# Optimization experiments

Hardware: AMD Instinct MI355X
Metric: run time of the kernel (lower is better)

Reference implementation:

```python
import jax, jax.numpy as jnp
import numpy as np

E = 320000          # num edges
G = 256             # num graphs
NNF = 128           # node features
NEF = 64            # edge features
NGF = 64            # global features
HID = 128           # hidden channels
TGT = 64            # num targets
IN_CH = 2 * NNF + NEF + NGF  # 384


def setup_inputs() -> dict:
    key = jax.random.key(0)
    ks = jax.random.split(key, 10)
    ek = jax.random.normal(ks[0], (E, NEF), dtype=jnp.float32)
    vrk = jax.random.normal(ks[1], (E, NNF), dtype=jnp.float32)
    vsk = jax.random.normal(ks[2], (E, NNF), dtype=jnp.float32)
    u = jax.random.normal(ks[3], (G, NGF), dtype=jnp.float32)
    batch = jnp.sort(jax.random.randint(ks[4], (E,), 0, G, dtype=jnp.int64))
    # MLP params (Linear stores weight [out, in]; we keep [in, out] for x @ W)
    s1 = 1.0 / np.sqrt(IN_CH)
    s2 = 1.0 / np.sqrt(HID)
    W1 = jax.random.uniform(ks[5], (IN_CH, HID), jnp.float32, -s1, s1)
    b1 = jax.random.uniform(ks[6], (HID,), jnp.float32, -s1, s1)
    W2 = jax.random.uniform(ks[7], (HID, TGT), jnp.float32, -s2, s2)
    b2 = jax.random.uniform(ks[8], (TGT,), jnp.float32, -s2, s2)
    return {"ek": ek, "vrk": vrk, "vsk": vsk, "u": u, "batch": batch,
            "W1": W1, "b1": b1, "W2": W2, "b2": b2}


def reference(ek, vrk, vsk, u, batch, W1, b1, W2, b2):
    # gather per-edge global features, concat, 2-layer MLP with ReLU
    x = jnp.concatenate([ek, vrk, vsk, u[batch]], axis=1)  # [E, IN_CH]
    h = jax.nn.relu(x @ W1 + b1)                           # [E, HID]
    return h @ W2 + b2                                     # [E, TGT]
```

## Files before the change

kernel.cpp:

```cpp
#include <hip/hip_runtime.h>
#include <hip/hip_bf16.h>
#include <stdint.h>


typedef __bf16 bf16;
typedef __attribute__((ext_vector_type(8))) __bf16 bf16x8;
typedef __attribute__((ext_vector_type(4))) __bf16 bf16x4;
typedef __attribute__((ext_vector_type(4))) float floatx4;

__device__ __forceinline__ bf16x8 cvt_b8(floatx4 a, floatx4 b) {
  bf16x8 r;
  r[0] = (bf16)a.x; r[1] = (bf16)a.y; r[2] = (bf16)a.z; r[3] = (bf16)a.w;
  r[4] = (bf16)b.x; r[5] = (bf16)b.y; r[6] = (bf16)b.z; r[7] = (bf16)b.w;
  return r;
}
__device__ __forceinline__ bf16x4 cvt_b4(floatx4 v) {
  bf16x4 r;
  r[0] = (bf16)v.x; r[1] = (bf16)v.y; r[2] = (bf16)v.z; r[3] = (bf16)v.w;
  return r;
}

__global__ void pack_pre(const float* __restrict__ W1, bf16* __restrict__ w1p,
                         const float* __restrict__ W2, bf16* __restrict__ w2p) {
  int b = blockIdx.x, lane = threadIdx.x;
  int mm = lane & 15, qq = lane >> 4;
  if (b < 96) {
    int kc = b >> 3, hf = b & 7;
    bf16x8 r;
    #pragma unroll
    for (int j = 0; j < 8; ++j)
      r[j] = (bf16)W1[(kc * 32 + qq * 8 + j) * 128 + hf * 16 + mm];
    *(bf16x8*)(w1p + ((long)b * 64 + lane) * 8) = r;
  } else {
    int bb = b - 96;
    int ks = bb >> 2, tf = bb & 3;
    bf16x8 r;
    #pragma unroll
    for (int j = 0; j < 8; ++j)
      r[j] = (bf16)W2[(ks * 32 + qq * 8 + j) * 64 + tf * 16 + mm];
    *(bf16x8*)(w2p + ((long)bb * 64 + lane) * 8) = r;
  }
}

__global__ __launch_bounds__(256, 4) void edge_mlp(
    const float* __restrict__ ek, const float* __restrict__ vrk, const float* __restrict__ vsk,
    const float* __restrict__ u, const int* __restrict__ batch,
    const bf16* __restrict__ w1p, const float* __restrict__ b1,
    const bf16* __restrict__ w2p, const float* __restrict__ b2,
    float* __restrict__ out)
{
  __shared__ __align__(16) bf16 smem[16384];
  const int tid  = threadIdx.x;
  const int lane = tid & 63;
  const int wv   = tid >> 6;
  const int m    = lane & 15;
  const int q    = lane >> 4;
  bf16* hs = smem + wv * 4096;

  const int e0 = blockIdx.x * 128 + wv * 32;

  const float* px[4][2];
  #pragma unroll
  for (int ef = 0; ef < 2; ++ef) {
    int e = e0 + ef * 16 + m;
    px[0][ef] = ek  + (long)e * 64  + q * 8;
    px[1][ef] = vrk + (long)e * 128 + q * 8;
    px[2][ef] = vsk + (long)e * 128 + q * 8;
    px[3][ef] = u   + (long)batch[e] * 64 + q * 8;
  }
  const bf16* wp = w1p + lane * 8;

  floatx4 acc[8][2] = {};
  #pragma unroll
  for (int kc = 0; kc < 12; ++kc) {
    const int src = (kc < 2) ? 0 : (kc < 6) ? 1 : (kc < 10) ? 2 : 3;
    const int off = (kc < 2) ? kc * 32
                  : (kc < 6) ? (kc - 2) * 32
                  : (kc < 10) ? (kc - 6) * 32 : (kc - 10) * 32;
    bf16x8 xb[2];
    #pragma unroll
    for (int ef = 0; ef < 2; ++ef) {
      floatx4 v0 = *(const floatx4*)(px[src][ef] + off);
      floatx4 v1 = *(const floatx4*)(px[src][ef] + off + 4);
      xb[ef] = cvt_b8(v0, v1);
    }
    #pragma unroll
    for (int hf = 0; hf < 8; ++hf) {
      bf16x8 af = *(const bf16x8*)(wp + (kc * 8 + hf) * 512);
      acc[hf][0] = __builtin_amdgcn_mfma_f32_16x16x32_bf16(af, xb[0], acc[hf][0], 0, 0, 0);
      acc[hf][1] = __builtin_amdgcn_mfma_f32_16x16x32_bf16(af, xb[1], acc[hf][1], 0, 0, 0);
    }
  }

  #pragma unroll
  for (int hf = 0; hf < 8; ++hf) {
    floatx4 b1v = *(const floatx4*)(b1 + hf * 16 + q * 4);
    #pragma unroll
    for (int ef = 0; ef < 2; ++ef) {
      floatx4 v = acc[hf][ef] + b1v;
      v.x = v.x > 0.f ? v.x : 0.f;
      v.y = v.y > 0.f ? v.y : 0.f;
      v.z = v.z > 0.f ? v.z : 0.f;
      v.w = v.w > 0.f ? v.w : 0.f;
      int r_e  = ef * 16 + m;
      int c    = hf * 2 + (q >> 1);
      int phys = c ^ (r_e & 15);
      *(bf16x4*)(hs + r_e * 128 + phys * 8 + (q & 1) * 4) = cvt_b4(v);
    }
  }
  asm volatile("s_waitcnt lgkmcnt(0)" ::: "memory");
  __builtin_amdgcn_sched_barrier(0);

  floatx4 acc2[4][2] = {};
  const bf16* wq = w2p + lane * 8;
  #pragma unroll
  for (int ks = 0; ks < 4; ++ks) {
    bf16x8 hb[2];
    #pragma unroll
    for (int ef = 0; ef < 2; ++ef) {
      int r_e  = ef * 16 + m;
      int phys = (ks * 4 + q) ^ (r_e & 15);
      hb[ef] = *(const bf16x8*)(hs + r_e * 128 + phys * 8);
    }
    #pragma unroll
    for (int tf = 0; tf < 4; ++tf) {
      bf16x8 a2 = *(const bf16x8*)(wq + (ks * 4 + tf) * 512);
      acc2[tf][0] = __builtin_amdgcn_mfma_f32_16x16x32_bf16(a2, hb[0], acc2[tf][0], 0, 0, 0);
      acc2[tf][1] = __builtin_amdgcn_mfma_f32_16x16x32_bf16(a2, hb[1], acc2[tf][1], 0, 0, 0);
    }
  }

  asm volatile("s_waitcnt lgkmcnt(0)" ::: "memory");
  __builtin_amdgcn_sched_barrier(0);
  float* fs = (float*)hs;
  #pragma unroll
  for (int tf = 0; tf < 4; ++tf) {
    floatx4 b2v = *(const floatx4*)(b2 + tf * 16 + q * 4);
    #pragma unroll
    for (int ef = 0; ef < 2; ++ef) {
      floatx4 v = acc2[tf][ef] + b2v;
      int r_e  = ef * 16 + m;
      int c    = tf * 4 + q;
      int phys = c ^ (r_e & 15);
      *(floatx4*)(fs + r_e * 64 + phys * 4) = v;
    }
  }
  asm volatile("s_waitcnt lgkmcnt(0)" ::: "memory");
  __builtin_amdgcn_sched_barrier(0);

  float* outp = out + (long)e0 * 64;
  #pragma unroll
  for (int i = 0; i < 8; ++i) {
    int r_e  = i * 4 + q;
    int phys = m ^ (r_e & 15);
    floatx4 v = *(const floatx4*)(fs + r_e * 64 + phys * 4);
    *(floatx4*)(outp + i * 256 + lane * 4) = v;
  }
}

extern "C" void kernel_launch(void* const* d_in, const int* in_sizes, int n_in,
                              void* d_out, int out_size, void* d_ws, size_t ws_size,
                              hipStream_t stream) {
  const float* ek    = (const float*)d_in[0];
  const float* vrk   = (const float*)d_in[1];
  const float* vsk   = (const float*)d_in[2];
  const float* u     = (const float*)d_in[3];
  const int*   batch = (const int*)d_in[4];
  const float* W1    = (const float*)d_in[5];
  const float* b1    = (const float*)d_in[6];
  const float* W2    = (const float*)d_in[7];
  const float* b2    = (const float*)d_in[8];
  float* out = (float*)d_out;

  bf16* w1p = (bf16*)d_ws;
  bf16* w2p = (bf16*)d_ws + 49152;

  pack_pre<<<112, 64, 0, stream>>>(W1, w1p, W2, w2p);
  edge_mlp<<<2500, 256, 0, stream>>>(ek, vrk, vsk, u, batch, w1p, b1, w2p, b2, out);
}
```

Baseline: 469.7 us.

## Stream edge inputs through double-buffered LDS via async global-to-LDS loads

Replaces direct per-lane global loads of the concatenated input rows with asynchronous global_load_lds transfers into a per-wave double-buffered, XOR-swizzled LDS region. The next K-chunk is prefetched while the current chunk's MFMAs run, and W1 fragments for each chunk plus all W2 fragments are loaded into registers up front. The aim is to hide global memory latency and get fully coalesced row loads, at the cost of doubled LDS per block and a lower occupancy target (3 blocks per CU instead of 4). The hand-coded vmcnt waits depend on exact counts of outstanding loads, including the W1 register loads.

```diff
diff --git a/kernel.cpp b/kernel.cpp
--- a/kernel.cpp
+++ b/kernel.cpp
@@ -7,6 +7,12 @@
 typedef __attribute__((ext_vector_type(8))) __bf16 bf16x8;
 typedef __attribute__((ext_vector_type(4))) __bf16 bf16x4;
 typedef __attribute__((ext_vector_type(4))) float floatx4;
+
+__device__ __forceinline__ void ldg2lds16(const void* g, void* l) {
+  __builtin_amdgcn_global_load_lds((__attribute__((address_space(1))) void*)g,
+                                   (__attribute__((address_space(3))) void*)l,
+                                   16, 0, 0);
+}
 
 __device__ __forceinline__ bf16x8 cvt_b8(floatx4 a, floatx4 b) {
   bf16x8 r;
@@ -42,56 +48,80 @@
   }
 }
 
-__global__ __launch_bounds__(256, 4) void edge_mlp(
+__global__ __launch_bounds__(256, 3) void edge_mlp(
     const float* __restrict__ ek, const float* __restrict__ vrk, const float* __restrict__ vsk,
     const float* __restrict__ u, const int* __restrict__ batch,
     const bf16* __restrict__ w1p, const float* __restrict__ b1,
     const bf16* __restrict__ w2p, const float* __restrict__ b2,
     float* __restrict__ out)
 {
-  __shared__ __align__(16) bf16 smem[16384];
+  __shared__ __align__(16) char smem[32768];
   const int tid  = threadIdx.x;
   const int lane = tid & 63;
   const int wv   = tid >> 6;
   const int m    = lane & 15;
   const int q    = lane >> 4;
-  bf16* hs = smem + wv * 4096;
+  char* wsl = smem + wv * 8192;
 
   const int e0 = blockIdx.x * 128 + wv * 32;
-
-  const float* px[4][2];
-  #pragma unroll
-  for (int ef = 0; ef < 2; ++ef) {
-    int e = e0 + ef * 16 + m;
-    px[0][ef] = ek  + (long)e * 64  + q * 8;
-    px[1][ef] = vrk + (long)e * 128 + q * 8;
-    px[2][ef] = vsk + (long)e * 128 + q * 8;
-    px[3][ef] = u   + (long)batch[e] * 64 + q * 8;
-  }
+  const int rl = lane >> 3;
+  const int cswz = ((lane & 7) ^ rl) * 16;
+
+  int ubr[4];
+  #pragma unroll
+  for (int i = 0; i < 4; ++i) ubr[i] = batch[e0 + i * 8 + rl];
+
+  const char* cek = (const char*)ek  + (long)e0 * 256;
+  const char* cvr = (const char*)vrk + (long)e0 * 512;
+  const char* cvs = (const char*)vsk + (long)e0 * 512;
+  const char* cu_ = (const char*)u;
+
+  auto stage = [&](int kc, int bufoff) {
+    #pragma unroll
+    for (int i = 0; i < 4; ++i) {
+      int r = i * 8 + rl;
+      const char* src;
+      if (kc < 2)       src = cek + (long)r * 256 + kc * 128 + cswz;
+      else if (kc < 6)  src = cvr + (long)r * 512 + (kc - 2) * 128 + cswz;
+      else if (kc < 10) src = cvs + (long)r * 512 + (kc - 6) * 128 + cswz;
+      else              src = cu_ + (long)ubr[i] * 256 + (kc - 10) * 128 + cswz;
+      ldg2lds16(src, wsl + bufoff + i * 1024);
+    }
+  };
+
   const bf16* wp = w1p + lane * 8;
-
+  const int off0 = ((q << 1) ^ (m & 7)) * 16;
+
+  stage(0, 0);
   floatx4 acc[8][2] = {};
   #pragma unroll
   for (int kc = 0; kc < 12; ++kc) {
-    const int src = (kc < 2) ? 0 : (kc < 6) ? 1 : (kc < 10) ? 2 : 3;
-    const int off = (kc < 2) ? kc * 32
-                  : (kc < 6) ? (kc - 2) * 32
-                  : (kc < 10) ? (kc - 6) * 32 : (kc - 10) * 32;
-    bf16x8 xb[2];
-    #pragma unroll
-    for (int ef = 0; ef < 2; ++ef) {
-      floatx4 v0 = *(const floatx4*)(px[src][ef] + off);
-      floatx4 v1 = *(const floatx4*)(px[src][ef] + off + 4);
-      xb[ef] = cvt_b8(v0, v1);
+    const int curoff = (kc & 1) * 4096;
+    bf16x8 wr[8];
+    #pragma unroll
+    for (int hf = 0; hf < 8; ++hf)
+      wr[hf] = *(const bf16x8*)(wp + (kc * 8 + hf) * 512);
+    if (kc < 11) stage(kc + 1, curoff ^ 4096);
+    __builtin_amdgcn_sched_barrier(0);
+    if (kc < 11) asm volatile("s_waitcnt vmcnt(12)" ::: "memory");
+    else         asm volatile("s_waitcnt vmcnt(8)"  ::: "memory");
+    __builtin_amdgcn_sched_barrier(0);
+    bf16x8 xv[2];
+    #pragma unroll
+    for (int ef = 0; ef < 2; ++ef) {
+      const char* p = wsl + curoff + (ef * 16 + m) * 128;
+      floatx4 lo = *(const floatx4*)(p + off0);
+      floatx4 hi = *(const floatx4*)(p + (off0 ^ 16));
+      xv[ef] = cvt_b8(lo, hi);
     }
     #pragma unroll
     for (int hf = 0; hf < 8; ++hf) {
-      bf16x8 af = *(const bf16x8*)(wp + (kc * 8 + hf) * 512);
-      acc[hf][0] = __builtin_amdgcn_mfma_f32_16x16x32_bf16(af, xb[0], acc[hf][0], 0, 0, 0);
-      acc[hf][1] = __builtin_amdgcn_mfma_f32_16x16x32_bf16(af, xb[1], acc[hf][1], 0, 0, 0);
-    }
-  }
-
+      acc[hf][0] = __builtin_amdgcn_mfma_f32_16x16x32_bf16(wr[hf], xv[0], acc[hf][0], 0, 0, 0);
+      acc[hf][1] = __builtin_amdgcn_mfma_f32_16x16x32_bf16(wr[hf], xv[1], acc[hf][1], 0, 0, 0);
+    }
+  }
+
+  bf16* hsp = (bf16*)wsl;
   #pragma unroll
   for (int hf = 0; hf < 8; ++hf) {
     floatx4 b1v = *(const floatx4*)(b1 + hf * 16 + q * 4);
@@ -105,7 +135,7 @@
       int r_e  = ef * 16 + m;
       int c    = hf * 2 + (q >> 1);
       int phys = c ^ (r_e & 15);
-      *(bf16x4*)(hs + r_e * 128 + phys * 8 + (q & 1) * 4) = cvt_b4(v);
+      *(bf16x4*)(hsp + r_e * 128 + phys * 8 + (q & 1) * 4) = cvt_b4(v);
     }
   }
   asm volatile("s_waitcnt lgkmcnt(0)" ::: "memory");
@@ -113,6 +143,9 @@
 
   floatx4 acc2[4][2] = {};
   const bf16* wq = w2p + lane * 8;
+  bf16x8 w2r[16];
+  #pragma unroll
+  for (int f = 0; f < 16; ++f) w2r[f] = *(const bf16x8*)(wq + f * 512);
   #pragma unroll
   for (int ks = 0; ks < 4; ++ks) {
     bf16x8 hb[2];
@@ -120,19 +153,18 @@
     for (int ef = 0; ef < 2; ++ef) {
       int r_e  = ef * 16 + m;
       int phys = (ks * 4 + q) ^ (r_e & 15);
-      hb[ef] = *(const bf16x8*)(hs + r_e * 128 + phys * 8);
+      hb[ef] = *(const bf16x8*)(hsp + r_e * 128 + phys * 8);
     }
     #pragma unroll
     for (int tf = 0; tf < 4; ++tf) {
-      bf16x8 a2 = *(const bf16x8*)(wq + (ks * 4 + tf) * 512);
-      acc2[tf][0] = __builtin_amdgcn_mfma_f32_16x16x32_bf16(a2, hb[0], acc2[tf][0], 0, 0, 0);
-      acc2[tf][1] = __builtin_amdgcn_mfma_f32_16x16x32_bf16(a2, hb[1], acc2[tf][1], 0, 0, 0);
+      acc2[tf][0] = __builtin_amdgcn_mfma_f32_16x16x32_bf16(w2r[ks * 4 + tf], hb[0], acc2[tf][0], 0, 0, 0);
+      acc2[tf][1] = __builtin_amdgcn_mfma_f32_16x16x32_bf16(w2r[ks * 4 + tf], hb[1], acc2[tf][1], 0, 0, 0);
     }
   }
 
   asm volatile("s_waitcnt lgkmcnt(0)" ::: "memory");
   __builtin_amdgcn_sched_barrier(0);
-  float* fs = (float*)hs;
+  float* fs = (float*)wsl;
   #pragma unroll
   for (int tf = 0; tf < 4; ++tf) {
     floatx4 b2v = *(const floatx4*)(b2 + tf * 16 + q * 4);
```

Result: faster. 425.0 us (-9.5%).
